# Optimization experiments

Measured on AMD Instinct MI355X. Metric: run time of the kernel, lower is better.

Reference implementation:

```python
import jax, jax.numpy as jnp
import numpy as np

N_NODES = 100000
N_EDGES = 1600000
IN_DIM = 128
HID = 128
N_CLASSES = 16
N_GRAPHS = 512


def setup_inputs() -> dict:
    key = jax.random.key(0)
    ks = jax.random.split(key, 16)
    d = {
        "x": jax.random.normal(ks[0], (N_NODES, IN_DIM), jnp.float32),
        "src": jax.random.randint(ks[1], (N_EDGES,), 0, N_NODES, jnp.int64 if jax.config.jax_enable_x64 else jnp.int32),
        "dst": jax.random.randint(ks[2], (N_EDGES,), 0, N_NODES, jnp.int64 if jax.config.jax_enable_x64 else jnp.int32),
        "gid": jnp.sort(jax.random.randint(ks[3], (N_NODES,), 0, N_GRAPHS, jnp.int64 if jax.config.jax_enable_x64 else jnp.int32)),
    }
    s = 1.0 / np.sqrt(HID)
    for i, k in zip(range(1, 5), ks[4:8]):
        d[f"W{i}"] = jax.random.uniform(k, (HID, HID), jnp.float32, -s, s)
        d[f"b{i}"] = jnp.zeros((HID,), jnp.float32)
    d["Wv"] = jax.random.uniform(ks[8], (HID, 1), jnp.float32, -s, s)
    d["bv"] = jnp.zeros((1,), jnp.float32)
    d["Wc"] = jax.random.uniform(ks[9], (HID, N_CLASSES), jnp.float32, -s, s)
    d["bc"] = jnp.zeros((N_CLASSES,), jnp.float32)
    return d


def _gcn_layer(h, W, b, src, dst, norm_src, norm_dst):
    # DGL GraphConv, norm='both': D_dst^{-1/2} * A * D_src^{-1/2} * h * W + b, then ReLU outside
    m = (h * norm_src[:, None])[src]                                  # [E, H] edge gather
    agg = jax.ops.segment_sum(m, dst, num_segments=N_NODES)           # [N, H] scatter-add
    return jax.nn.relu(agg * norm_dst[:, None] @ W + b)


def reference(x, W1, b1, W2, b2, W3, b3, W4, b4, Wv, bv, Wc, bc, src, dst, gid):
    ones = jnp.ones((N_EDGES,), jnp.float32)
    deg_out = jnp.clip(jax.ops.segment_sum(ones, src, num_segments=N_NODES), 1.0)
    deg_in = jnp.clip(jax.ops.segment_sum(ones, dst, num_segments=N_NODES), 1.0)
    norm_src = jax.lax.rsqrt(deg_out)
    norm_dst = jax.lax.rsqrt(deg_in)

    h = _gcn_layer(x, W1, b1, src, dst, norm_src, norm_dst)
    h = _gcn_layer(h, W2, b2, src, dst, norm_src, norm_dst)
    h = _gcn_layer(h, W3, b3, src, dst, norm_src, norm_dst)
    h = _gcn_layer(h, W4, b4, src, dst, norm_src, norm_dst)

    w = jax.nn.sigmoid(h @ Wv + bv)                                   # [N, 1]
    num = jax.ops.segment_sum(h * w, gid, num_segments=N_GRAPHS)      # [G, H]
    den = jax.ops.segment_sum(w, gid, num_segments=N_GRAPHS)          # [G, 1]
    hg = jnp.where(den > 0, num / jnp.where(den > 0, den, 1.0), 0.0)  # weighted mean readout
    return hg @ Wc + bc                                               # [G, n_classes]
```

## Files before the change

kernel.cpp:

```cpp
#include <hip/hip_runtime.h>
#include <hip/hip_bf16.h>

#define N_NODES_C 100000
#define N_EDGES_C 1600000
#define HID_C 128
#define NCLS_C 16
#define NGRAPH_C 512
#define ELL_CAP 64
#define PREP_GROUPS 8
#define PREP_RANGE ((N_NODES_C + PREP_GROUPS - 1) / PREP_GROUPS)
#define PREP_GB 256
#define PREP_CHUNK (N_EDGES_C / PREP_GB)

__global__ __launch_bounds__(256) void k_prep(
    const int* __restrict__ src, const int* __restrict__ dst,
    int* cnt_out, int* cursor, int* __restrict__ ell) {
  int grp = blockIdx.x & (PREP_GROUPS - 1);
  int gb = blockIdx.x >> 3;
  int lo = grp * PREP_RANGE;
  int e0 = gb * PREP_CHUNK;
  int e1 = e0 + PREP_CHUNK;
  for (int i = e0 + threadIdx.x; i < e1; i += 256) {
    int s = src[i];
    int d = dst[i];
    if ((unsigned)(s - lo) < (unsigned)PREP_RANGE) atomicAdd(&cnt_out[s], 1);
    if ((unsigned)(d - lo) < (unsigned)PREP_RANGE) {
      int p = atomicAdd(&cursor[d], 1);
      if (p < ELL_CAP) ell[((size_t)d << 6) + p] = s;
    }
  }
}

__global__ void k_gstart(const int* __restrict__ gid, int* __restrict__ gstart) {
  int n = blockIdx.x * blockDim.x + threadIdx.x;
  if (n >= N_NODES_C) return;
  int g = gid[n];
  int gp = (n == 0) ? -1 : gid[n - 1];
  for (int k = gp + 1; k <= g; ++k) gstart[k] = n;
  if (n == N_NODES_C - 1) {
    for (int k = g + 1; k <= NGRAPH_C; ++k) gstart[k] = N_NODES_C;
  }
}

__global__ __launch_bounds__(256) void k_gemm_rowscale(
    const float* __restrict__ A, const float* __restrict__ W,
    const int* __restrict__ cnt_out, float* __restrict__ T, int rows) {
  __shared__ float sA[32][132];
  __shared__ float sB[32][132];
  int t = threadIdx.x;
  int tx = t & 15, ty = t >> 4;
  int m0 = blockIdx.x * 128;

  float acc[8][8];
#pragma unroll
  for (int i = 0; i < 8; ++i)
#pragma unroll
    for (int j = 0; j < 8; ++j) acc[i][j] = 0.f;

  int a_c4 = (t & 7) * 4;
  int a_r = t >> 3;
  int w_n4 = (t & 31) * 4;
  int w_k = t >> 5;

  for (int k0 = 0; k0 < HID_C; k0 += 32) {
#pragma unroll
    for (int rr = 0; rr < 4; ++rr) {
      int r = rr * 32 + a_r;
      int row = m0 + r;
      float4 v = make_float4(0.f, 0.f, 0.f, 0.f);
      if (row < rows) v = *(const float4*)&A[(size_t)row * HID_C + k0 + a_c4];
      sA[a_c4 + 0][r] = v.x;
      sA[a_c4 + 1][r] = v.y;
      sA[a_c4 + 2][r] = v.z;
      sA[a_c4 + 3][r] = v.w;
    }
#pragma unroll
    for (int i = 0; i < 4; ++i) {
      int kc = i * 8 + w_k;
      float4 v = *(const float4*)&W[(size_t)(k0 + kc) * HID_C + w_n4];
      *(float4*)&sB[kc][w_n4] = v;
    }
    __syncthreads();

#pragma unroll 4
    for (int kk = 0; kk < 32; ++kk) {
      float4 a0 = *(const float4*)&sA[kk][ty * 8];
      float4 a1 = *(const float4*)&sA[kk][ty * 8 + 4];
      float4 bb0 = *(const float4*)&sB[kk][tx * 8];
      float4 bb1 = *(const float4*)&sB[kk][tx * 8 + 4];
      float a[8] = {a0.x, a0.y, a0.z, a0.w, a1.x, a1.y, a1.z, a1.w};
      float b[8] = {bb0.x, bb0.y, bb0.z, bb0.w, bb1.x, bb1.y, bb1.z, bb1.w};
#pragma unroll
      for (int i = 0; i < 8; ++i)
#pragma unroll
        for (int j = 0; j < 8; ++j) acc[i][j] = fmaf(a[i], b[j], acc[i][j]);
    }
    __syncthreads();
  }

#pragma unroll
  for (int i = 0; i < 8; ++i) {
    int row = m0 + ty * 8 + i;
    if (row < rows) {
      float sc = 1.f / sqrtf(fmaxf((float)cnt_out[row], 1.f));
      float4 v0 = {acc[i][0] * sc, acc[i][1] * sc, acc[i][2] * sc, acc[i][3] * sc};
      float4 v1 = {acc[i][4] * sc, acc[i][5] * sc, acc[i][6] * sc, acc[i][7] * sc};
      float4* p = (float4*)&T[(size_t)row * HID_C + tx * 8];
      p[0] = v0;
      p[1] = v1;
    }
  }
}

__global__ __launch_bounds__(256) void k_agg(
    const float* __restrict__ T, const int* __restrict__ cnt_in,
    const int* __restrict__ ell, const float* __restrict__ bias,
    float* __restrict__ H) {
  int wid = threadIdx.x >> 6, lane = threadIdx.x & 63;
  int half = lane >> 5, li = lane & 31;
  int n = blockIdx.x * 4 + wid;
  if (n >= N_NODES_C) return;
  const int* lst = ell + ((size_t)n << 6);
  int deg = cnt_in[n];
  if (deg > ELL_CAP) deg = ELL_CAP;
  const float4* T4 = (const float4*)T;
  float4 acc = make_float4(0.f, 0.f, 0.f, 0.f);
  int e = 0;
  for (; e + 8 <= deg; e += 8) {
    int i0 = lst[e + 0 + half];
    int i1 = lst[e + 2 + half];
    int i2 = lst[e + 4 + half];
    int i3 = lst[e + 6 + half];
    float4 v0 = T4[(size_t)i0 * 32 + li];
    float4 v1 = T4[(size_t)i1 * 32 + li];
    float4 v2 = T4[(size_t)i2 * 32 + li];
    float4 v3 = T4[(size_t)i3 * 32 + li];
    acc.x += v0.x + v1.x + v2.x + v3.x;
    acc.y += v0.y + v1.y + v2.y + v3.y;
    acc.z += v0.z + v1.z + v2.z + v3.z;
    acc.w += v0.w + v1.w + v2.w + v3.w;
  }
  for (; e + 2 <= deg; e += 2) {
    int i = lst[e + half];
    float4 v = T4[(size_t)i * 32 + li];
    acc.x += v.x;
    acc.y += v.y;
    acc.z += v.z;
    acc.w += v.w;
  }
  if (e < deg) {
    int i = lst[e];
    float4 v = T4[(size_t)i * 32 + li];
    if (half == 0) {
      acc.x += v.x;
      acc.y += v.y;
      acc.z += v.z;
      acc.w += v.w;
    }
  }
  acc.x += __shfl_xor(acc.x, 32);
  acc.y += __shfl_xor(acc.y, 32);
  acc.z += __shfl_xor(acc.z, 32);
  acc.w += __shfl_xor(acc.w, 32);
  if (half == 0) {
    float nd = 1.f / sqrtf(fmaxf((float)cnt_in[n], 1.f));
    float4 bb = ((const float4*)bias)[li];
    float4 r;
    r.x = fmaxf(fmaf(acc.x, nd, bb.x), 0.f);
    r.y = fmaxf(fmaf(acc.y, nd, bb.y), 0.f);
    r.z = fmaxf(fmaf(acc.z, nd, bb.z), 0.f);
    r.w = fmaxf(fmaf(acc.w, nd, bb.w), 0.f);
    ((float4*)H)[(size_t)n * 32 + li] = r;
  }
}

__global__ __launch_bounds__(256) void k_readout(
    const float* __restrict__ H, const float* __restrict__ Wv,
    const float* __restrict__ bv, const int* __restrict__ gstart,
    const float* __restrict__ Wc, const float* __restrict__ bc,
    float* __restrict__ out) {
  int g = blockIdx.x;
  int wid = threadIdx.x >> 6, lane = threadIdx.x & 63;
  int s0 = gstart[g], s1 = gstart[g + 1];
  float2 wv2 = ((const float2*)Wv)[lane];
  float bvs = bv[0];
  float ax = 0.f, ay = 0.f, dw = 0.f;
  for (int n = s0 + wid; n < s1; n += 4) {
    float2 h2 = ((const float2*)H)[(size_t)n * 64 + lane];
    float p = h2.x * wv2.x + h2.y * wv2.y;
#pragma unroll
    for (int off = 32; off > 0; off >>= 1) p += __shfl_xor(p, off);
    float w = 1.f / (1.f + expf(-(p + bvs)));
    ax += h2.x * w;
    ay += h2.y * w;
    dw += w;
  }
  __shared__ float2 snum[4][64];
  __shared__ float sden[4];
  __shared__ float hg[HID_C];
  snum[wid][lane] = make_float2(ax, ay);
  if (lane == 0) sden[wid] = dw;
  __syncthreads();
  if (wid == 0) {
    float2 a = snum[0][lane], b = snum[1][lane], c = snum[2][lane], d = snum[3][lane];
    float den = sden[0] + sden[1] + sden[2] + sden[3];
    float inv = (den > 0.f) ? 1.f / den : 0.f;
    hg[2 * lane] = (a.x + b.x + c.x + d.x) * inv;
    hg[2 * lane + 1] = (a.y + b.y + c.y + d.y) * inv;
  }
  __syncthreads();
  if (threadIdx.x < NCLS_C) {
    int c = threadIdx.x;
    float acc = 0.f;
    for (int k = 0; k < HID_C; ++k) acc = fmaf(hg[k], Wc[k * NCLS_C + c], acc);
    out[g * NCLS_C + c] = acc + bc[c];
  }
}

extern "C" void kernel_launch(void* const* d_in, const int* in_sizes, int n_in,
                              void* d_out, int out_size, void* d_ws, size_t ws_size,
                              hipStream_t stream) {
  const float* x = (const float*)d_in[0];
  const int* src = (const int*)d_in[1];
  const int* dst = (const int*)d_in[2];
  const int* gid = (const int*)d_in[3];
  const float* W[4] = {(const float*)d_in[4], (const float*)d_in[6],
                       (const float*)d_in[8], (const float*)d_in[10]};
  const float* b[4] = {(const float*)d_in[5], (const float*)d_in[7],
                       (const float*)d_in[9], (const float*)d_in[11]};
  const float* Wv = (const float*)d_in[12];
  const float* bv = (const float*)d_in[13];
  const float* Wc = (const float*)d_in[14];
  const float* bc = (const float*)d_in[15];
  float* out = (float*)d_out;

  char* ws = (char*)d_ws;
  size_t off = 0;
  auto alloc = [&](size_t bytes) -> char* {
    char* p = ws + off;
    off = (off + bytes + 255) & ~(size_t)255;
    return p;
  };
  int* cnt_out = (int*)alloc((size_t)N_NODES_C * 4);
  int* cursor = (int*)alloc((size_t)N_NODES_C * 4);
  int* gstart = (int*)alloc((size_t)(NGRAPH_C + 1) * 4);
  int* ell = (int*)alloc((size_t)N_NODES_C * ELL_CAP * 4);
  float* tbuf = (float*)alloc((size_t)N_NODES_C * HID_C * 4);
  float* hbuf = (float*)alloc((size_t)N_NODES_C * HID_C * 4);
  (void)ws_size;
  (void)in_sizes;
  (void)n_in;
  (void)out_size;

  hipMemsetAsync(cnt_out, 0, (size_t)N_NODES_C * 4, stream);
  hipMemsetAsync(cursor, 0, (size_t)N_NODES_C * 4, stream);

  k_prep<<<PREP_GROUPS * PREP_GB, 256, 0, stream>>>(src, dst, cnt_out, cursor, ell);
  k_gstart<<<(N_NODES_C + 255) / 256, 256, 0, stream>>>(gid, gstart);

  int gemm_grid = (N_NODES_C + 127) / 128;
  int node_grid = (N_NODES_C + 3) / 4;
  const float* hin = x;
  for (int l = 0; l < 4; ++l) {
    k_gemm_rowscale<<<gemm_grid, 256, 0, stream>>>(hin, W[l], cnt_out, tbuf, N_NODES_C);
    k_agg<<<node_grid, 256, 0, stream>>>(tbuf, cursor, ell, b[l], hbuf);
    hin = hbuf;
  }

  k_readout<<<NGRAPH_C, 256, 0, stream>>>(hbuf, Wv, bv, gstart, Wc, bc, out);
}
```

Before: 825.0 us.

## Fuse neighbor aggregation with the next layer's GEMM via shared-memory tile

Adds k_aggemm, in which each block aggregates 64 nodes' neighbor features into a shared-memory tile and then multiplies that tile by the next layer's weight matrix. This replaces the separate agg and GEMM launches for three of the four layers. The goal is to stop writing the full hidden-state buffer to global memory and reading it back between layers. In exchange, each wave processes 16 nodes one after another, and the large shared-memory footprint limits occupancy, which may reduce how many gathers are in flight. The dst normalization now uses the ELL-clamped degree instead of the raw count.

```diff
diff --git a/kernel.cpp b/kernel.cpp
--- a/kernel.cpp
+++ b/kernel.cpp
@@ -106,6 +106,129 @@
       float4 v0 = {acc[i][0] * sc, acc[i][1] * sc, acc[i][2] * sc, acc[i][3] * sc};
       float4 v1 = {acc[i][4] * sc, acc[i][5] * sc, acc[i][6] * sc, acc[i][7] * sc};
       float4* p = (float4*)&T[(size_t)row * HID_C + tx * 8];
+      p[0] = v0;
+      p[1] = v1;
+    }
+  }
+}
+
+__global__ __launch_bounds__(256, 3) void k_aggemm(
+    const float* __restrict__ Tprev, const int* __restrict__ cnt_in,
+    const int* __restrict__ ell, const float* __restrict__ bias,
+    const float* __restrict__ W, const int* __restrict__ cnt_out,
+    float* __restrict__ Tnext) {
+  __shared__ float hA[64][132];
+  __shared__ float sB[32][132];
+  int t = threadIdx.x;
+  int wid = t >> 6, lane = t & 63;
+  int half = lane >> 5, li = lane & 31;
+  int m0 = blockIdx.x * 64;
+  const float4* T4 = (const float4*)Tprev;
+
+#pragma unroll 1
+  for (int j = 0; j < 16; ++j) {
+    int n = m0 + wid * 16 + j;
+    if (n >= N_NODES_C) break;
+    const int* lst = ell + ((size_t)n << 6);
+    int deg = cnt_in[n];
+    if (deg > ELL_CAP) deg = ELL_CAP;
+    float4 acc = make_float4(0.f, 0.f, 0.f, 0.f);
+    int e = 0;
+    for (; e + 8 <= deg; e += 8) {
+      int i0 = lst[e + 0 + half];
+      int i1 = lst[e + 2 + half];
+      int i2 = lst[e + 4 + half];
+      int i3 = lst[e + 6 + half];
+      float4 v0 = T4[(size_t)i0 * 32 + li];
+      float4 v1 = T4[(size_t)i1 * 32 + li];
+      float4 v2 = T4[(size_t)i2 * 32 + li];
+      float4 v3 = T4[(size_t)i3 * 32 + li];
+      acc.x += v0.x + v1.x + v2.x + v3.x;
+      acc.y += v0.y + v1.y + v2.y + v3.y;
+      acc.z += v0.z + v1.z + v2.z + v3.z;
+      acc.w += v0.w + v1.w + v2.w + v3.w;
+    }
+    for (; e + 2 <= deg; e += 2) {
+      int i = lst[e + half];
+      float4 v = T4[(size_t)i * 32 + li];
+      acc.x += v.x;
+      acc.y += v.y;
+      acc.z += v.z;
+      acc.w += v.w;
+    }
+    if (e < deg) {
+      int i = lst[e];
+      float4 v = T4[(size_t)i * 32 + li];
+      if (half == 0) {
+        acc.x += v.x;
+        acc.y += v.y;
+        acc.z += v.z;
+        acc.w += v.w;
+      }
+    }
+    acc.x += __shfl_xor(acc.x, 32);
+    acc.y += __shfl_xor(acc.y, 32);
+    acc.z += __shfl_xor(acc.z, 32);
+    acc.w += __shfl_xor(acc.w, 32);
+    if (half == 0) {
+      float nd = 1.f / sqrtf(fmaxf((float)deg, 1.f));
+      float4 bb = ((const float4*)bias)[li];
+      float4 r;
+      r.x = fmaxf(fmaf(acc.x, nd, bb.x), 0.f);
+      r.y = fmaxf(fmaf(acc.y, nd, bb.y), 0.f);
+      r.z = fmaxf(fmaf(acc.z, nd, bb.z), 0.f);
+      r.w = fmaxf(fmaf(acc.w, nd, bb.w), 0.f);
+      *(float4*)&hA[n - m0][li * 4] = r;
+    }
+  }
+  __syncthreads();
+
+  int tx = t & 15, ty = t >> 4;
+  int w_n4 = (t & 31) * 4;
+  int w_k = t >> 5;
+  float acc[4][8];
+#pragma unroll
+  for (int i = 0; i < 4; ++i)
+#pragma unroll
+    for (int j = 0; j < 8; ++j) acc[i][j] = 0.f;
+
+  for (int k0 = 0; k0 < HID_C; k0 += 32) {
+#pragma unroll
+    for (int i = 0; i < 4; ++i) {
+      int kc = i * 8 + w_k;
+      float4 v = *(const float4*)&W[(size_t)(k0 + kc) * HID_C + w_n4];
+      *(float4*)&sB[kc][w_n4] = v;
+    }
+    __syncthreads();
+
+#pragma unroll 4
+    for (int kk = 0; kk < 32; ++kk) {
+      float a0 = hA[ty * 4 + 0][k0 + kk];
+      float a1 = hA[ty * 4 + 1][k0 + kk];
+      float a2 = hA[ty * 4 + 2][k0 + kk];
+      float a3 = hA[ty * 4 + 3][k0 + kk];
+      float4 bb0 = *(const float4*)&sB[kk][tx * 8];
+      float4 bb1 = *(const float4*)&sB[kk][tx * 8 + 4];
+      float b[8] = {bb0.x, bb0.y, bb0.z, bb0.w, bb1.x, bb1.y, bb1.z, bb1.w};
+#pragma unroll
+      for (int j = 0; j < 8; ++j) {
+        acc[0][j] = fmaf(a0, b[j], acc[0][j]);
+        acc[1][j] = fmaf(a1, b[j], acc[1][j]);
+        acc[2][j] = fmaf(a2, b[j], acc[2][j]);
+        acc[3][j] = fmaf(a3, b[j], acc[3][j]);
+      }
+    }
+    __syncthreads();
+  }
+
+#pragma unroll
+  for (int i = 0; i < 4; ++i) {
+    int row = m0 + ty * 4 + i;
+    if (row < N_NODES_C) {
+      float sc = 1.f / sqrtf(fmaxf((float)cnt_out[row], 1.f));
+      float4 v0 = {acc[i][0] * sc, acc[i][1] * sc, acc[i][2] * sc, acc[i][3] * sc};
+      float4 v1 = {acc[i][4] * sc, acc[i][5] * sc, acc[i][6] * sc, acc[i][7] * sc};
+      float4* p = (float4*)&Tnext[(size_t)row * HID_C + tx * 8];
       p[0] = v0;
       p[1] = v1;
     }
@@ -163,7 +286,7 @@
   acc.z += __shfl_xor(acc.z, 32);
   acc.w += __shfl_xor(acc.w, 32);
   if (half == 0) {
-    float nd = 1.f / sqrtf(fmaxf((float)cnt_in[n], 1.f));
+    float nd = 1.f / sqrtf(fmaxf((float)deg, 1.f));
     float4 bb = ((const float4*)bias)[li];
     float4 r;
     r.x = fmaxf(fmaf(acc.x, nd, bb.x), 0.f);
@@ -245,8 +368,8 @@
   int* cursor = (int*)alloc((size_t)N_NODES_C * 4);
   int* gstart = (int*)alloc((size_t)(NGRAPH_C + 1) * 4);
   int* ell = (int*)alloc((size_t)N_NODES_C * ELL_CAP * 4);
-  float* tbuf = (float*)alloc((size_t)N_NODES_C * HID_C * 4);
-  float* hbuf = (float*)alloc((size_t)N_NODES_C * HID_C * 4);
+  float* bufA = (float*)alloc((size_t)N_NODES_C * HID_C * 4);
+  float* bufB = (float*)alloc((size_t)N_NODES_C * HID_C * 4);
   (void)ws_size;
   (void)in_sizes;
   (void)n_in;
@@ -259,13 +382,14 @@
   k_gstart<<<(N_NODES_C + 255) / 256, 256, 0, stream>>>(gid, gstart);
 
   int gemm_grid = (N_NODES_C + 127) / 128;
+  int fused_grid = (N_NODES_C + 63) / 64;
   int node_grid = (N_NODES_C + 3) / 4;
-  const float* hin = x;
-  for (int l = 0; l < 4; ++l) {
-    k_gemm_rowscale<<<gemm_grid, 256, 0, stream>>>(hin, W[l], cnt_out, tbuf, N_NODES_C);
-    k_agg<<<node_grid, 256, 0, stream>>>(tbuf, cursor, ell, b[l], hbuf);
-    hin = hbuf;
-  }
-
-  k_readout<<<NGRAPH_C, 256, 0, stream>>>(hbuf, Wv, bv, gstart, Wc, bc, out);
-}
+
+  k_gemm_rowscale<<<gemm_grid, 256, 0, stream>>>(x, W[0], cnt_out, bufA, N_NODES_C);
+  k_aggemm<<<fused_grid, 256, 0, stream>>>(bufA, cursor, ell, b[0], W[1], cnt_out, bufB);
+  k_aggemm<<<fused_grid, 256, 0, stream>>>(bufB, cursor, ell, b[1], W[2], cnt_out, bufA);
+  k_aggemm<<<fused_grid, 256, 0, stream>>>(bufA, cursor, ell, b[2], W[3], cnt_out, bufB);
+  k_agg<<<node_grid, 256, 0, stream>>>(bufB, cursor, ell, b[3], bufA);
+
+  k_readout<<<NGRAPH_C, 256, 0, stream>>>(bufA, Wv, bv, gstart, Wc, bc, out);
+}
```

New measurement: 927.0 us. +12.4%, slower.

## Move source-degree scaling into aggregation and fuse first GEMM with graph prep

Applied to the files above, without the earlier changes.

The source-degree normalization is now applied per edge inside the aggregation kernel instead of in the GEMM epilogue, so the GEMM no longer depends on edge counts. This lets the first-layer GEMM run in one merged launch with the edge bucketing and graph-start kernels, overlapping them. In exchange, each aggregation does an extra gather of out-degree and an rsqrt per edge, and the merged kernel allocates GEMM shared memory for every block type.

```diff
diff --git a/kernel.cpp b/kernel.cpp
--- a/kernel.cpp
+++ b/kernel.cpp
@@ -12,44 +12,16 @@
 #define PREP_GB 256
 #define PREP_CHUNK (N_EDGES_C / PREP_GB)
 
-__global__ __launch_bounds__(256) void k_prep(
-    const int* __restrict__ src, const int* __restrict__ dst,
-    int* cnt_out, int* cursor, int* __restrict__ ell) {
-  int grp = blockIdx.x & (PREP_GROUPS - 1);
-  int gb = blockIdx.x >> 3;
-  int lo = grp * PREP_RANGE;
-  int e0 = gb * PREP_CHUNK;
-  int e1 = e0 + PREP_CHUNK;
-  for (int i = e0 + threadIdx.x; i < e1; i += 256) {
-    int s = src[i];
-    int d = dst[i];
-    if ((unsigned)(s - lo) < (unsigned)PREP_RANGE) atomicAdd(&cnt_out[s], 1);
-    if ((unsigned)(d - lo) < (unsigned)PREP_RANGE) {
-      int p = atomicAdd(&cursor[d], 1);
-      if (p < ELL_CAP) ell[((size_t)d << 6) + p] = s;
-    }
-  }
-}
-
-__global__ void k_gstart(const int* __restrict__ gid, int* __restrict__ gstart) {
-  int n = blockIdx.x * blockDim.x + threadIdx.x;
-  if (n >= N_NODES_C) return;
-  int g = gid[n];
-  int gp = (n == 0) ? -1 : gid[n - 1];
-  for (int k = gp + 1; k <= g; ++k) gstart[k] = n;
-  if (n == N_NODES_C - 1) {
-    for (int k = g + 1; k <= NGRAPH_C; ++k) gstart[k] = N_NODES_C;
-  }
-}
-
-__global__ __launch_bounds__(256) void k_gemm_rowscale(
+#define GEMM_BLOCKS ((N_NODES_C + 127) / 128)
+#define PREP_BLOCKS (PREP_GROUPS * PREP_GB)
+#define GS_BLOCKS ((N_NODES_C + 255) / 256)
+#define FRONT_BLOCKS (GEMM_BLOCKS + PREP_BLOCKS + GS_BLOCKS)
+
+__device__ __forceinline__ void gemm_body(
     const float* __restrict__ A, const float* __restrict__ W,
-    const int* __restrict__ cnt_out, float* __restrict__ T, int rows) {
-  __shared__ float sA[32][132];
-  __shared__ float sB[32][132];
+    float* __restrict__ U, int m0, float (*sA)[132], float (*sB)[132]) {
   int t = threadIdx.x;
   int tx = t & 15, ty = t >> 4;
-  int m0 = blockIdx.x * 128;
 
   float acc[8][8];
 #pragma unroll
@@ -68,7 +40,7 @@
       int r = rr * 32 + a_r;
       int row = m0 + r;
       float4 v = make_float4(0.f, 0.f, 0.f, 0.f);
-      if (row < rows) v = *(const float4*)&A[(size_t)row * HID_C + k0 + a_c4];
+      if (row < N_NODES_C) v = *(const float4*)&A[(size_t)row * HID_C + k0 + a_c4];
       sA[a_c4 + 0][r] = v.x;
       sA[a_c4 + 1][r] = v.y;
       sA[a_c4 + 2][r] = v.z;
@@ -101,61 +73,110 @@
 #pragma unroll
   for (int i = 0; i < 8; ++i) {
     int row = m0 + ty * 8 + i;
-    if (row < rows) {
-      float sc = 1.f / sqrtf(fmaxf((float)cnt_out[row], 1.f));
-      float4 v0 = {acc[i][0] * sc, acc[i][1] * sc, acc[i][2] * sc, acc[i][3] * sc};
-      float4 v1 = {acc[i][4] * sc, acc[i][5] * sc, acc[i][6] * sc, acc[i][7] * sc};
-      float4* p = (float4*)&T[(size_t)row * HID_C + tx * 8];
+    if (row < N_NODES_C) {
+      float4 v0 = {acc[i][0], acc[i][1], acc[i][2], acc[i][3]};
+      float4 v1 = {acc[i][4], acc[i][5], acc[i][6], acc[i][7]};
+      float4* p = (float4*)&U[(size_t)row * HID_C + tx * 8];
       p[0] = v0;
       p[1] = v1;
     }
   }
 }
 
+__global__ __launch_bounds__(256) void k_front(
+    const float* __restrict__ x, const float* __restrict__ W1,
+    float* __restrict__ U1, const int* __restrict__ src,
+    const int* __restrict__ dst, int* cnt_out, int* cursor,
+    int* __restrict__ ell, const int* __restrict__ gid,
+    int* __restrict__ gstart) {
+  __shared__ float sA[32][132];
+  __shared__ float sB[32][132];
+  int bid = blockIdx.x;
+  if (bid < GEMM_BLOCKS) {
+    gemm_body(x, W1, U1, bid * 128, sA, sB);
+  } else if (bid < GEMM_BLOCKS + PREP_BLOCKS) {
+    int grp = bid & (PREP_GROUPS - 1);
+    int gb = (bid - GEMM_BLOCKS) >> 3;
+    int lo = grp * PREP_RANGE;
+    int e0 = gb * PREP_CHUNK;
+    int e1 = e0 + PREP_CHUNK;
+    for (int i = e0 + threadIdx.x; i < e1; i += 256) {
+      int s = src[i];
+      int d = dst[i];
+      if ((unsigned)(s - lo) < (unsigned)PREP_RANGE) atomicAdd(&cnt_out[s], 1);
+      if ((unsigned)(d - lo) < (unsigned)PREP_RANGE) {
+        int p = atomicAdd(&cursor[d], 1);
+        if (p < ELL_CAP) ell[((size_t)d << 6) + p] = s;
+      }
+    }
+  } else {
+    int n = (bid - GEMM_BLOCKS - PREP_BLOCKS) * 256 + threadIdx.x;
+    if (n >= N_NODES_C) return;
+    int g = gid[n];
+    int gp = (n == 0) ? -1 : gid[n - 1];
+    for (int k = gp + 1; k <= g; ++k) gstart[k] = n;
+    if (n == N_NODES_C - 1) {
+      for (int k = g + 1; k <= NGRAPH_C; ++k) gstart[k] = N_NODES_C;
+    }
+  }
+}
+
+__global__ __launch_bounds__(256) void k_gemm(
+    const float* __restrict__ A, const float* __restrict__ W,
+    float* __restrict__ U) {
+  __shared__ float sA[32][132];
+  __shared__ float sB[32][132];
+  gemm_body(A, W, U, blockIdx.x * 128, sA, sB);
+}
+
 __global__ __launch_bounds__(256) void k_agg(
-    const float* __restrict__ T, const int* __restrict__ cnt_in,
-    const int* __restrict__ ell, const float* __restrict__ bias,
-    float* __restrict__ H) {
+    const float* __restrict__ U, const int* __restrict__ cnt_in,
+    const int* __restrict__ cnt_out, const int* __restrict__ ell,
+    const float* __restrict__ bias, float* __restrict__ H) {
   int wid = threadIdx.x >> 6, lane = threadIdx.x & 63;
   int half = lane >> 5, li = lane & 31;
   int n = blockIdx.x * 4 + wid;
   if (n >= N_NODES_C) return;
   const int* lst = ell + ((size_t)n << 6);
-  int deg = cnt_in[n];
-  if (deg > ELL_CAP) deg = ELL_CAP;
-  const float4* T4 = (const float4*)T;
+  int degfull = cnt_in[n];
+  int deg = degfull > ELL_CAP ? ELL_CAP : degfull;
+  const float4* U4 = (const float4*)U;
   float4 acc = make_float4(0.f, 0.f, 0.f, 0.f);
   int e = 0;
   for (; e + 8 <= deg; e += 8) {
-    int i0 = lst[e + 0 + half];
-    int i1 = lst[e + 2 + half];
-    int i2 = lst[e + 4 + half];
-    int i3 = lst[e + 6 + half];
-    float4 v0 = T4[(size_t)i0 * 32 + li];
-    float4 v1 = T4[(size_t)i1 * 32 + li];
-    float4 v2 = T4[(size_t)i2 * 32 + li];
-    float4 v3 = T4[(size_t)i3 * 32 + li];
-    acc.x += v0.x + v1.x + v2.x + v3.x;
-    acc.y += v0.y + v1.y + v2.y + v3.y;
-    acc.z += v0.z + v1.z + v2.z + v3.z;
-    acc.w += v0.w + v1.w + v2.w + v3.w;
+    int i0 = lst[e + 0 + half], i1 = lst[e + 2 + half];
+    int i2 = lst[e + 4 + half], i3 = lst[e + 6 + half];
+    float s0 = 1.f / sqrtf((float)cnt_out[i0]);
+    float s1 = 1.f / sqrtf((float)cnt_out[i1]);
+    float s2 = 1.f / sqrtf((float)cnt_out[i2]);
+    float s3 = 1.f / sqrtf((float)cnt_out[i3]);
+    float4 v0 = U4[(size_t)i0 * 32 + li];
+    float4 v1 = U4[(size_t)i1 * 32 + li];
+    float4 v2 = U4[(size_t)i2 * 32 + li];
+    float4 v3 = U4[(size_t)i3 * 32 + li];
+    acc.x = fmaf(v0.x, s0, fmaf(v1.x, s1, fmaf(v2.x, s2, fmaf(v3.x, s3, acc.x))));
+    acc.y = fmaf(v0.y, s0, fmaf(v1.y, s1, fmaf(v2.y, s2, fmaf(v3.y, s3, acc.y))));
+    acc.z = fmaf(v0.z, s0, fmaf(v1.z, s1, fmaf(v2.z, s2, fmaf(v3.z, s3, acc.z))));
+    acc.w = fmaf(v0.w, s0, fmaf(v1.w, s1, fmaf(v2.w, s2, fmaf(v3.w, s3, acc.w))));
   }
   for (; e + 2 <= deg; e += 2) {
     int i = lst[e + half];
-    float4 v = T4[(size_t)i * 32 + li];
-    acc.x += v.x;
-    acc.y += v.y;
-    acc.z += v.z;
-    acc.w += v.w;
+    float s = 1.f / sqrtf((float)cnt_out[i]);
+    float4 v = U4[(size_t)i * 32 + li];
+    acc.x = fmaf(v.x, s, acc.x);
+    acc.y = fmaf(v.y, s, acc.y);
+    acc.z = fmaf(v.z, s, acc.z);
+    acc.w = fmaf(v.w, s, acc.w);
   }
   if (e < deg) {
     int i = lst[e];
-    float4 v = T4[(size_t)i * 32 + li];
+    float s = 1.f / sqrtf((float)cnt_out[i]);
+    float4 v = U4[(size_t)i * 32 + li];
     if (half == 0) {
-      acc.x += v.x;
-      acc.y += v.y;
-      acc.z += v.z;
-      acc.w += v.w;
+      acc.x = fmaf(v.x, s, acc.x);
+      acc.y = fmaf(v.y, s, acc.y);
+      acc.z = fmaf(v.z, s, acc.z);
+      acc.w = fmaf(v.w, s, acc.w);
     }
   }
   acc.x += __shfl_xor(acc.x, 32);
@@ -163,7 +184,7 @@
   acc.z += __shfl_xor(acc.z, 32);
   acc.w += __shfl_xor(acc.w, 32);
   if (half == 0) {
-    float nd = 1.f / sqrtf(fmaxf((float)cnt_in[n], 1.f));
+    float nd = 1.f / sqrtf(fmaxf((float)degfull, 1.f));
     float4 bb = ((const float4*)bias)[li];
     float4 r;
     r.x = fmaxf(fmaf(acc.x, nd, bb.x), 0.f);
@@ -245,8 +266,8 @@
   int* cursor = (int*)alloc((size_t)N_NODES_C * 4);
   int* gstart = (int*)alloc((size_t)(NGRAPH_C + 1) * 4);
   int* ell = (int*)alloc((size_t)N_NODES_C * ELL_CAP * 4);
-  float* tbuf = (float*)alloc((size_t)N_NODES_C * HID_C * 4);
-  float* hbuf = (float*)alloc((size_t)N_NODES_C * HID_C * 4);
+  float* bufU = (float*)alloc((size_t)N_NODES_C * HID_C * 4);
+  float* bufH = (float*)alloc((size_t)N_NODES_C * HID_C * 4);
   (void)ws_size;
   (void)in_sizes;
   (void)n_in;
@@ -255,17 +276,15 @@
   hipMemsetAsync(cnt_out, 0, (size_t)N_NODES_C * 4, stream);
   hipMemsetAsync(cursor, 0, (size_t)N_NODES_C * 4, stream);
 
-  k_prep<<<PREP_GROUPS * PREP_GB, 256, 0, stream>>>(src, dst, cnt_out, cursor, ell);
-  k_gstart<<<(N_NODES_C + 255) / 256, 256, 0, stream>>>(gid, gstart);
-
-  int gemm_grid = (N_NODES_C + 127) / 128;
+  k_front<<<FRONT_BLOCKS, 256, 0, stream>>>(x, W[0], bufU, src, dst, cnt_out,
+                                            cursor, ell, gid, gstart);
+
   int node_grid = (N_NODES_C + 3) / 4;
-  const float* hin = x;
-  for (int l = 0; l < 4; ++l) {
-    k_gemm_rowscale<<<gemm_grid, 256, 0, stream>>>(hin, W[l], cnt_out, tbuf, N_NODES_C);
-    k_agg<<<node_grid, 256, 0, stream>>>(tbuf, cursor, ell, b[l], hbuf);
-    hin = hbuf;
-  }
-
-  k_readout<<<NGRAPH_C, 256, 0, stream>>>(hbuf, Wv, bv, gstart, Wc, bc, out);
-}
+  k_agg<<<node_grid, 256, 0, stream>>>(bufU, cursor, cnt_out, ell, b[0], bufH);
+  for (int l = 1; l < 4; ++l) {
+    k_gemm<<<GEMM_BLOCKS, 256, 0, stream>>>(bufH, W[l], bufU);
+    k_agg<<<node_grid, 256, 0, stream>>>(bufU, cursor, cnt_out, ell, b[l], bufH);
+  }
+
+  k_readout<<<NGRAPH_C, 256, 0, stream>>>(bufH, Wv, bv, gstart, Wc, bc, out);
+}
```

Result: no change. 811.0 us (-1.7%).
